# Kernel tuning notes

Hardware: AMD Instinct MI355X
Metric: run time of the kernel (lower is better)

The kernel has to match this reference:

```python
import jax, jax.numpy as jnp
import numpy as np

BATCH, N_FEATURES, D_MODEL = 8192, 8192, 1024


def setup_inputs() -> dict:
    key = jax.random.key(0)
    kx, kw = jax.random.split(key)
    # x: sparse feature activations in the original (COO); dense uniform here.
    x = jax.random.uniform(kx, (BATCH, N_FEATURES), dtype=jnp.float32)
    # Xavier-normal init for W_tr [n_features, d_model].
    std = float(np.sqrt(2.0 / (N_FEATURES + D_MODEL)))
    W_tr = jax.random.normal(kw, (N_FEATURES, D_MODEL), dtype=jnp.float32) * std
    bias = jnp.zeros((N_FEATURES,), dtype=jnp.float32)
    return {"x": x, "W_tr": W_tr, "bias": bias}


def reference(x, W_tr, bias):
    # h = x @ W_tr              : [B, n_features] @ [n_features, d_model] -> [B, d_model]
    # out = relu(h @ W_tr.T + b): [B, d_model] @ [d_model, n_features] -> [B, n_features]
    h = jnp.einsum("bf,fd->bd", x, W_tr)
    return jax.nn.relu(jnp.einsum("bd,fd->bf", h, W_tr) + bias)
```

## Files before the change

### kernel.cpp

```cpp
#include <hip/hip_runtime.h>
#include <hip/hip_bf16.h>
#include <stdint.h>

#define BATCH  8192
#define NFEAT  8192
#define DMODEL 1024

typedef unsigned short u16;
typedef __attribute__((ext_vector_type(8))) short  short8;
typedef __attribute__((ext_vector_type(4))) float  f32x4;

__device__ __forceinline__ u16 f2b(float f) {
    uint32_t u = __float_as_uint(f);
    u += 0x7fffu + ((u >> 16) & 1u);
    return (u16)(u >> 16);
}

__device__ __forceinline__ void gld16(const u16* g, void* l) {
    __builtin_amdgcn_global_load_lds(
        (const __attribute__((address_space(1))) void*)(uintptr_t)g,
        (__attribute__((address_space(3))) void*)(uint32_t)(uintptr_t)l,
        16, 0, 0);
}


__global__ void cvt_x_kernel(const float* __restrict__ x, u16* __restrict__ xb) {
    int i = blockIdx.x * blockDim.x + threadIdx.x;
    const float4* xv = (const float4*)x;
    float4 a = xv[2 * i];
    float4 b = xv[2 * i + 1];
    union { u16 u[8]; uint4 v; } o;
    o.u[0] = f2b(a.x); o.u[1] = f2b(a.y); o.u[2] = f2b(a.z); o.u[3] = f2b(a.w);
    o.u[4] = f2b(b.x); o.u[5] = f2b(b.y); o.u[6] = f2b(b.z); o.u[7] = f2b(b.w);
    ((uint4*)xb)[i] = o.v;
}

__global__ void cvt_w_kernel(const float* __restrict__ W,
                             u16* __restrict__ wb, u16* __restrict__ wt) {
    __shared__ u16 tile[64][65];
    const int f0 = blockIdx.x * 64;
    const int d0 = blockIdx.y * 64;
    const int t  = threadIdx.x;
#pragma unroll
    for (int rep = 0; rep < 16; ++rep) {
        int idx = rep * 256 + t;
        int r = idx >> 6, c = idx & 63;
        float v = W[(size_t)(f0 + r) * DMODEL + d0 + c];
        u16 u = f2b(v);
        tile[r][c] = u;
        wb[(size_t)(f0 + r) * DMODEL + d0 + c] = u;
    }
    __syncthreads();
#pragma unroll
    for (int rep = 0; rep < 16; ++rep) {
        int idx = rep * 256 + t;
        int r = idx >> 6, c = idx & 63;
        wt[(size_t)(d0 + r) * NFEAT + f0 + c] = tile[c][r];
    }
}

#define SYNC_IN()  do { __builtin_amdgcn_s_barrier(); \
                        asm volatile("s_waitcnt lgkmcnt(0)" ::: "memory"); } while (0)
#define SYNC_OUT() do { __builtin_amdgcn_s_setprio(0); __builtin_amdgcn_s_barrier(); } while (0)

__global__ __launch_bounds__(512, 2)
void gemm1_2ph(const u16* __restrict__ A, const u16* __restrict__ B,
               u16* __restrict__ H, int N, int K) {
    const int NT = K >> 6;
    __shared__ __align__(1024) char lds[131072];
    const int BOFF = 98304;

    const int tid  = threadIdx.x;
    const int lane = tid & 63;
    const int wave = tid >> 6;
    const int wm   = wave >> 2;
    const int wn   = wave & 3;

    const int nwg = gridDim.x;
    const int swz = (blockIdx.x & 7) * (nwg >> 3) + (blockIdx.x >> 3);
    const int ntn = N >> 7;
    const int tm0 = (swz / ntn) << 8;
    const int tn0 = (swz % ntn) << 7;

    const int srl = lane >> 2;
    const int sch = (lane & 3) ^ (((lane >> 5) & 1) << 1);
    const int scol  = (wave & 1) * 32 + sch * 8;
    const int srow0 = (wave >> 1) * 16 + srl;

    const u16* pa[2][2];
    pa[0][0] = A + (size_t)(tm0 + srow0)            * K + scol;
    pa[0][1] = A + (size_t)(tm0 + srow0 + 64)       * K + scol;
    pa[1][0] = A + (size_t)(tm0 + 128 + srow0)      * K + scol;
    pa[1][1] = A + (size_t)(tm0 + 128 + srow0 + 64) * K + scol;
    const u16* pb[2];
    pb[0] = B + (size_t)(tn0 + srow0)      * K + scol;
    pb[1] = B + (size_t)(tn0 + srow0 + 64) * K + scol;

    auto STAGE_A = [&](int tau, int half) {
        if (tau < NT) {
            char* d = lds + (tau % 3) * 32768 + half * 16384 + wave * 1024;
            gld16(pa[half][0] + (size_t)tau * 64, d);
            gld16(pa[half][1] + (size_t)tau * 64, d + 8192);
        }
    };
    auto STAGE_B = [&](int tau) {
        if (tau < NT) {
            char* d = lds + BOFF + (tau & 1) * 16384 + wave * 1024;
            gld16(pb[0] + (size_t)tau * 64, d);
            gld16(pb[1] + (size_t)tau * 64, d + 8192);
        }
    };

    const int l15 = lane & 15, lhi = lane >> 4;
    const int pch = lhi ^ (((lane >> 3) & 1) << 1);
    const int lof = l15 * 64 + pch * 16;

    short8 a[4][2];
    short8 b[2][2];
    f32x4  acc[8][2] = {};

    const char* Ab;
    const char* Bb;
    auto LDA_ = [&](int mh) {
#pragma unroll
        for (int fm = 0; fm < 4; ++fm)
#pragma unroll
            for (int ks = 0; ks < 2; ++ks)
                a[fm][ks] = *(const short8*)(Ab + ((mh * 4 + fm) * 2 + ks) * 1024);
    };
    auto LDB_ = [&](int nh) {
#pragma unroll
        for (int ks = 0; ks < 2; ++ks)
            b[nh][ks] = *(const short8*)(Bb + (nh * 2 + ks) * 1024);
    };
    auto MMA_ = [&](int mh, int nh) {
#pragma unroll
        for (int ks = 0; ks < 2; ++ks)
#pragma unroll
            for (int fm = 0; fm < 4; ++fm)
                acc[mh * 4 + fm][nh] = __builtin_amdgcn_mfma_f32_16x16x32_bf16(
                    a[fm][ks], b[nh][ks], acc[mh * 4 + fm][nh], 0, 0, 0);
    };

    STAGE_A(0, 0); STAGE_A(0, 1); STAGE_B(0);
    STAGE_A(1, 0); STAGE_A(1, 1); STAGE_B(1);
    asm volatile("s_waitcnt vmcnt(6)" ::: "memory");
    __builtin_amdgcn_s_barrier();

    for (int t = 0; t < NT; ++t) {
        Ab = lds + (t % 3) * 32768 + wm * 16384 + lof;
        Bb = lds + BOFF + (t & 1) * 16384 + wn * 4096 + lof;

        LDA_(0); LDB_(0); LDB_(1);
        STAGE_A(t + 2, 0);
        STAGE_A(t + 2, 1);
        SYNC_IN();
        __builtin_amdgcn_s_setprio(1);
        MMA_(0, 0);
        MMA_(0, 1);
        SYNC_OUT();

        LDA_(1);
        STAGE_B(t + 2);
        SYNC_IN();
        __builtin_amdgcn_s_setprio(1);
        MMA_(1, 1);
        MMA_(1, 0);
        __builtin_amdgcn_s_setprio(0);
        if (t < NT - 2)       asm volatile("s_waitcnt vmcnt(6)" ::: "memory");
        else if (t == NT - 2) asm volatile("s_waitcnt vmcnt(0)" ::: "memory");
        __builtin_amdgcn_s_barrier();
    }

    u16* lu = (u16*)lds;
#pragma unroll
    for (int fm = 0; fm < 8; ++fm)
#pragma unroll
        for (int nh = 0; nh < 2; ++nh) {
            const int col  = wn * 32 + nh * 16 + l15;
            const int row0 = wm * 128 + fm * 16 + lhi * 4;
#pragma unroll
            for (int r = 0; r < 4; ++r)
                lu[(row0 + r) * 128 + col] = f2b(acc[fm][nh][r]);
        }
    __syncthreads();
    const uint4* ls = (const uint4*)lds;
#pragma unroll
    for (int s = 0; s < 8; ++s) {
        int i = s * 512 + tid;
        int row = i >> 4;
        int col = (i & 15) * 8;
        *(uint4*)(H + (size_t)(tm0 + row) * N + (tn0 + col)) = ls[i];
    }
}

__global__ __launch_bounds__(512, 2)
void gemm2_persist(const u16* __restrict__ A, const u16* __restrict__ B,
                   float* __restrict__ O, const float* __restrict__ bias,
                   int N, int K) {
    __shared__ __align__(1024) char lds[163840];
    const int BOFF = 98304;
    const int TTOT = 64;

    const int tid  = threadIdx.x;
    const int lane = tid & 63;
    const int wave = tid >> 6;
    const int wm   = wave >> 2;
    const int wn   = wave & 3;

    const int bid = blockIdx.x;
    const int xcd = bid & 7;
    const int sub = (bid >> 3) & 3;
    const int mg  = bid >> 5;
    const int tn0     = ((xcd << 2) + sub) << 8;
    const int tm_base = mg << 10;

    const int srl = lane >> 2;
    const int sch = (lane & 3) ^ (((lane >> 5) & 1) << 1);
    const int scol  = (wave & 1) * 32 + sch * 8;
    const int srow0 = (wave >> 1) * 16 + srl;

    auto STAGE_A = [&](int tau, int half) {
        if (tau < TTOT) {
            char* d = lds + (tau % 3) * 32768 + half * 16384 + wave * 1024;
            const int rb = tm_base + ((tau >> 4) << 8) + half * 128 + srow0;
            const u16* p = A + (size_t)rb * K + ((tau & 15) << 6) + scol;
            gld16(p, d);
            gld16(p + (size_t)64 * K, d + 8192);
        }
    };
    auto STAGE_B = [&](int tau, int half) {
        if (tau < TTOT) {
            char* d = lds + BOFF + (tau & 1) * 32768 + half * 16384 + wave * 1024;
            const u16* p = B + (size_t)(tn0 + half * 128 + srow0) * K + ((tau & 15) << 6) + scol;
            gld16(p, d);
            gld16(p + (size_t)64 * K, d + 8192);
        }
    };

    const int l15 = lane & 15, lhi = lane >> 4;
    const int pch = lhi ^ (((lane >> 3) & 1) << 1);
    const int lof = l15 * 64 + pch * 16;

    short8 a[4][2];
    short8 b[4][2];
    f32x4  acc[8][4] = {};

    const char* Ab;
    const char* Bb;
    auto LDA_ = [&](int mh) {
#pragma unroll
        for (int fm = 0; fm < 4; ++fm)
#pragma unroll
            for (int ks = 0; ks < 2; ++ks)
                a[fm][ks] = *(const short8*)(Ab + ((mh * 4 + fm) * 2 + ks) * 1024);
    };
    auto LDB_ = [&](int nh) {
#pragma unroll
        for (int fn = 0; fn < 2; ++fn)
#pragma unroll
            for (int ks = 0; ks < 2; ++ks)
                b[nh * 2 + fn][ks] = *(const short8*)(Bb + (((wn & 1) * 4 + nh * 2 + fn) * 2 + ks) * 1024);
    };
    auto MMA_ = [&](int mh, int nh) {
#pragma unroll
        for (int ks = 0; ks < 2; ++ks)
#pragma unroll
            for (int fm = 0; fm < 4; ++fm)
#pragma unroll
                for (int fn = 0; fn < 2; ++fn)
                    acc[mh * 4 + fm][nh * 2 + fn] = __builtin_amdgcn_mfma_f32_16x16x32_bf16(
                        a[fm][ks], b[nh * 2 + fn][ks], acc[mh * 4 + fm][nh * 2 + fn], 0, 0, 0);
    };

    const int ocol = tn0 + wn * 64;
    float bv[4];
#pragma unroll
    for (int fn = 0; fn < 4; ++fn) bv[fn] = bias[ocol + fn * 16 + l15];

    STAGE_A(0, 0); STAGE_A(0, 1); STAGE_B(0, 0); STAGE_B(0, 1);
    STAGE_A(1, 0); STAGE_A(1, 1); STAGE_B(1, 0); STAGE_B(1, 1);
    asm volatile("s_waitcnt vmcnt(8)" ::: "memory");
    __builtin_amdgcn_s_barrier();

    for (int tt = 0; tt < TTOT; ++tt) {
        Ab = lds + (tt % 3) * 32768 + wm * 16384 + lof;
        Bb = lds + BOFF + (tt & 1) * 32768 + (wn >> 1) * 16384 + lof;

        LDA_(0); LDB_(0); LDB_(1);
        STAGE_A(tt + 2, 0);
        STAGE_A(tt + 2, 1);
        SYNC_IN();
        __builtin_amdgcn_s_setprio(1);
        MMA_(0, 0);
        MMA_(0, 1);
        SYNC_OUT();

        LDA_(1);
        STAGE_B(tt + 2, 0);
        STAGE_B(tt + 2, 1);
        SYNC_IN();
        __builtin_amdgcn_s_setprio(1);
        MMA_(1, 1);
        MMA_(1, 0);
        __builtin_amdgcn_s_setprio(0);
        if (tt < TTOT - 2)       asm volatile("s_waitcnt vmcnt(8)" ::: "memory");
        else if (tt == TTOT - 2) asm volatile("s_waitcnt vmcnt(0)" ::: "memory");
        __builtin_amdgcn_s_barrier();

        if ((tt & 15) == 15) {
            const int orow = tm_base + ((tt >> 4) << 8) + wm * 128;
#pragma unroll
            for (int fm = 0; fm < 8; ++fm) {
                const int row0 = orow + fm * 16 + lhi * 4;
#pragma unroll
                for (int fn = 0; fn < 4; ++fn) {
                    const int col = ocol + fn * 16 + l15;
#pragma unroll
                    for (int r = 0; r < 4; ++r) {
                        float v = acc[fm][fn][r] + bv[fn];
                        O[(size_t)(row0 + r) * N + col] = v > 0.f ? v : 0.f;
                        acc[fm][fn][r] = 0.f;
                    }
                }
            }
        }
    }
}


extern "C" void kernel_launch(void* const* d_in, const int* in_sizes, int n_in,
                              void* d_out, int out_size, void* d_ws, size_t ws_size,
                              hipStream_t stream) {
    const float* x    = (const float*)d_in[0];
    const float* W    = (const float*)d_in[1];
    const float* bias = (const float*)d_in[2];
    float* out = (float*)d_out;

    char* ws = (char*)d_ws;
    u16* xb = (u16*)ws;
    u16* wt = (u16*)(ws + 134217728);
    u16* wb = (u16*)(ws + 134217728 + 16777216);
    u16* hb = (u16*)(ws + 134217728 + 2 * 16777216);

    cvt_x_kernel<<<(BATCH * NFEAT / 8) / 256, 256, 0, stream>>>(x, xb);
    cvt_w_kernel<<<dim3(NFEAT / 64, DMODEL / 64), 256, 0, stream>>>(W, wb, wt);

    gemm1_2ph<<<dim3((BATCH / 256) * (DMODEL / 128)), 512, 0, stream>>>(
        xb, wt, hb, DMODEL, NFEAT);

    gemm2_persist<<<dim3(256), 512, 0, stream>>>(
        hb, wb, out, bias, NFEAT, DMODEL);
}
```

Measured before the change: 373.1 us.

## Restage GEMM tiles as full 128-byte rows with XOR-swizzled LDS chunks

Both GEMM kernels change how tiles are staged into LDS. Each group of 8 lanes now loads one full 64-element (128-byte) row per global-to-LDS load, instead of four lanes covering half a row. Rows are stored contiguously in LDS with the 16-byte chunk index XOR-swizzled by row, and the fragment reads use matching swizzled offsets. The aim is more coalesced global loads and bank-conflict-free LDS fragment reads, at the cost of different address arithmetic. The number of loads per stage is unchanged, so the vmcnt waits still match.

Result: no change. 379.0 us (+1.6%).

```diff
diff --git a/kernel.cpp b/kernel.cpp
--- a/kernel.cpp
+++ b/kernel.cpp
@@ -63,6 +63,7 @@
                         asm volatile("s_waitcnt lgkmcnt(0)" ::: "memory"); } while (0)
 #define SYNC_OUT() do { __builtin_amdgcn_s_setprio(0); __builtin_amdgcn_s_barrier(); } while (0)
 
+
 __global__ __launch_bounds__(512, 2)
 void gemm1_2ph(const u16* __restrict__ A, const u16* __restrict__ B,
                u16* __restrict__ H, int N, int K) {
@@ -82,38 +83,29 @@
     const int tm0 = (swz / ntn) << 8;
     const int tn0 = (swz % ntn) << 7;
 
-    const int srl = lane >> 2;
-    const int sch = (lane & 3) ^ (((lane >> 5) & 1) << 1);
-    const int scol  = (wave & 1) * 32 + sch * 8;
-    const int srow0 = (wave >> 1) * 16 + srl;
-
-    const u16* pa[2][2];
-    pa[0][0] = A + (size_t)(tm0 + srow0)            * K + scol;
-    pa[0][1] = A + (size_t)(tm0 + srow0 + 64)       * K + scol;
-    pa[1][0] = A + (size_t)(tm0 + 128 + srow0)      * K + scol;
-    pa[1][1] = A + (size_t)(tm0 + 128 + srow0 + 64) * K + scol;
-    const u16* pb[2];
-    pb[0] = B + (size_t)(tn0 + srow0)      * K + scol;
-    pb[1] = B + (size_t)(tn0 + srow0 + 64) * K + scol;
-
-    auto STAGE_A = [&](int tau, int half) {
+    const int sr8 = lane >> 3;
+    const int sg  = (lane & 7) ^ sr8;
+    const int l15 = lane & 15, lhi = lane >> 4;
+    const int ch0 = ((lhi ^ (lane & 7)) << 4);
+
+    auto STAGE_A = [&](int tau) {
         if (tau < NT) {
-            char* d = lds + (tau % 3) * 32768 + half * 16384 + wave * 1024;
-            gld16(pa[half][0] + (size_t)tau * 64, d);
-            gld16(pa[half][1] + (size_t)tau * 64, d + 8192);
+            char* d = lds + (tau % 3) * 32768 + wave * 4096;
+#pragma unroll
+            for (int i = 0; i < 4; ++i)
+                gld16(A + (size_t)(tm0 + wave * 32 + i * 8 + sr8) * K + ((size_t)tau << 6) + sg * 8,
+                      d + i * 1024);
         }
     };
     auto STAGE_B = [&](int tau) {
         if (tau < NT) {
-            char* d = lds + BOFF + (tau & 1) * 16384 + wave * 1024;
-            gld16(pb[0] + (size_t)tau * 64, d);
-            gld16(pb[1] + (size_t)tau * 64, d + 8192);
-        }
-    };
-
-    const int l15 = lane & 15, lhi = lane >> 4;
-    const int pch = lhi ^ (((lane >> 3) & 1) << 1);
-    const int lof = l15 * 64 + pch * 16;
+            char* d = lds + BOFF + (tau & 1) * 16384 + wave * 2048;
+#pragma unroll
+            for (int i = 0; i < 2; ++i)
+                gld16(B + (size_t)(tn0 + wave * 16 + i * 8 + sr8) * K + ((size_t)tau << 6) + sg * 8,
+                      d + i * 1024);
+        }
+    };
 
     short8 a[4][2];
     short8 b[2][2];
@@ -123,15 +115,14 @@
     const char* Bb;
     auto LDA_ = [&](int mh) {
 #pragma unroll
-        for (int fm = 0; fm < 4; ++fm)
-#pragma unroll
-            for (int ks = 0; ks < 2; ++ks)
-                a[fm][ks] = *(const short8*)(Ab + ((mh * 4 + fm) * 2 + ks) * 1024);
+        for (int fm = 0; fm < 4; ++fm) {
+            a[fm][0] = *(const short8*)(Ab + (mh * 4 + fm) * 2048 + ch0);
+            a[fm][1] = *(const short8*)(Ab + (mh * 4 + fm) * 2048 + (ch0 ^ 64));
+        }
     };
     auto LDB_ = [&](int nh) {
-#pragma unroll
-        for (int ks = 0; ks < 2; ++ks)
-            b[nh][ks] = *(const short8*)(Bb + (nh * 2 + ks) * 1024);
+        b[nh][0] = *(const short8*)(Bb + nh * 2048 + ch0);
+        b[nh][1] = *(const short8*)(Bb + nh * 2048 + (ch0 ^ 64));
     };
     auto MMA_ = [&](int mh, int nh) {
 #pragma unroll
@@ -142,18 +133,17 @@
                     a[fm][ks], b[nh][ks], acc[mh * 4 + fm][nh], 0, 0, 0);
     };
 
-    STAGE_A(0, 0); STAGE_A(0, 1); STAGE_B(0);
-    STAGE_A(1, 0); STAGE_A(1, 1); STAGE_B(1);
+    STAGE_A(0); STAGE_B(0);
+    STAGE_A(1); STAGE_B(1);
     asm volatile("s_waitcnt vmcnt(6)" ::: "memory");
     __builtin_amdgcn_s_barrier();
 
     for (int t = 0; t < NT; ++t) {
-        Ab = lds + (t % 3) * 32768 + wm * 16384 + lof;
-        Bb = lds + BOFF + (t & 1) * 16384 + wn * 4096 + lof;
+        Ab = lds + (t % 3) * 32768 + wm * 16384 + l15 * 128;
+        Bb = lds + BOFF + (t & 1) * 16384 + wn * 4096 + l15 * 128;
 
         LDA_(0); LDB_(0); LDB_(1);
-        STAGE_A(t + 2, 0);
-        STAGE_A(t + 2, 1);
+        STAGE_A(t + 2);
         SYNC_IN();
         __builtin_amdgcn_s_setprio(1);
         MMA_(0, 0);
@@ -215,32 +205,31 @@
     const int tn0     = ((xcd << 2) + sub) << 8;
     const int tm_base = mg << 10;
 
-    const int srl = lane >> 2;
-    const int sch = (lane & 3) ^ (((lane >> 5) & 1) << 1);
-    const int scol  = (wave & 1) * 32 + sch * 8;
-    const int srow0 = (wave >> 1) * 16 + srl;
-
-    auto STAGE_A = [&](int tau, int half) {
+    const int sr8 = lane >> 3;
+    const int sg  = (lane & 7) ^ sr8;
+    const int l15 = lane & 15, lhi = lane >> 4;
+    const int ch0 = ((lhi ^ (lane & 7)) << 4);
+
+    auto STAGE_A = [&](int tau) {
         if (tau < TTOT) {
-            char* d = lds + (tau % 3) * 32768 + half * 16384 + wave * 1024;
-            const int rb = tm_base + ((tau >> 4) << 8) + half * 128 + srow0;
-            const u16* p = A + (size_t)rb * K + ((tau & 15) << 6) + scol;
-            gld16(p, d);
-            gld16(p + (size_t)64 * K, d + 8192);
-        }
-    };
-    auto STAGE_B = [&](int tau, int half) {
+            char* d = lds + (tau % 3) * 32768 + wave * 4096;
+            const int rb = tm_base + ((tau >> 4) << 8) + wave * 32 + sr8;
+            const size_t co = ((size_t)(tau & 15) << 6) + sg * 8;
+#pragma unroll
+            for (int i = 0; i < 4; ++i)
+                gld16(A + (size_t)(rb + i * 8) * K + co, d + i * 1024);
+        }
+    };
+    auto STAGE_B = [&](int tau) {
         if (tau < TTOT) {
-            char* d = lds + BOFF + (tau & 1) * 32768 + half * 16384 + wave * 1024;
-            const u16* p = B + (size_t)(tn0 + half * 128 + srow0) * K + ((tau & 15) << 6) + scol;
-            gld16(p, d);
-            gld16(p + (size_t)64 * K, d + 8192);
-        }
-    };
-
-    const int l15 = lane & 15, lhi = lane >> 4;
-    const int pch = lhi ^ (((lane >> 3) & 1) << 1);
-    const int lof = l15 * 64 + pch * 16;
+            char* d = lds + BOFF + (tau & 1) * 32768 + wave * 4096;
+            const int rb = tn0 + wave * 32 + sr8;
+            const size_t co = ((size_t)(tau & 15) << 6) + sg * 8;
+#pragma unroll
+            for (int i = 0; i < 4; ++i)
+                gld16(B + (size_t)(rb + i * 8) * K + co, d + i * 1024);
+        }
+    };
 
     short8 a[4][2];
     short8 b[4][2];
@@ -250,17 +239,17 @@
     const char* Bb;
     auto LDA_ = [&](int mh) {
 #pragma unroll
-        for (int fm = 0; fm < 4; ++fm)
-#pragma unroll
-            for (int ks = 0; ks < 2; ++ks)
-                a[fm][ks] = *(const short8*)(Ab + ((mh * 4 + fm) * 2 + ks) * 1024);
+        for (int fm = 0; fm < 4; ++fm) {
+            a[fm][0] = *(const short8*)(Ab + (mh * 4 + fm) * 2048 + ch0);
+            a[fm][1] = *(const short8*)(Ab + (mh * 4 + fm) * 2048 + (ch0 ^ 64));
+        }
     };
     auto LDB_ = [&](int nh) {
 #pragma unroll
-        for (int fn = 0; fn < 2; ++fn)
-#pragma unroll
-            for (int ks = 0; ks < 2; ++ks)
-                b[nh * 2 + fn][ks] = *(const short8*)(Bb + (((wn & 1) * 4 + nh * 2 + fn) * 2 + ks) * 1024);
+        for (int fn = 0; fn < 2; ++fn) {
+            b[nh * 2 + fn][0] = *(const short8*)(Bb + (nh * 2 + fn) * 2048 + ch0);
+            b[nh * 2 + fn][1] = *(const short8*)(Bb + (nh * 2 + fn) * 2048 + (ch0 ^ 64));
+        }
     };
     auto MMA_ = [&](int mh, int nh) {
 #pragma unroll
@@ -278,18 +267,17 @@
 #pragma unroll
     for (int fn = 0; fn < 4; ++fn) bv[fn] = bias[ocol + fn * 16 + l15];
 
-    STAGE_A(0, 0); STAGE_A(0, 1); STAGE_B(0, 0); STAGE_B(0, 1);
-    STAGE_A(1, 0); STAGE_A(1, 1); STAGE_B(1, 0); STAGE_B(1, 1);
+    STAGE_A(0); STAGE_B(0);
+    STAGE_A(1); STAGE_B(1);
     asm volatile("s_waitcnt vmcnt(8)" ::: "memory");
     __builtin_amdgcn_s_barrier();
 
     for (int tt = 0; tt < TTOT; ++tt) {
-        Ab = lds + (tt % 3) * 32768 + wm * 16384 + lof;
-        Bb = lds + BOFF + (tt & 1) * 32768 + (wn >> 1) * 16384 + lof;
+        Ab = lds + (tt % 3) * 32768 + wm * 16384 + l15 * 128;
+        Bb = lds + BOFF + (tt & 1) * 32768 + wn * 8192 + l15 * 128;
 
         LDA_(0); LDB_(0); LDB_(1);
-        STAGE_A(tt + 2, 0);
-        STAGE_A(tt + 2, 1);
+        STAGE_A(tt + 2);
         SYNC_IN();
         __builtin_amdgcn_s_setprio(1);
         MMA_(0, 0);
@@ -297,8 +285,7 @@
         SYNC_OUT();
 
         LDA_(1);
-        STAGE_B(tt + 2, 0);
-        STAGE_B(tt + 2, 1);
+        STAGE_B(tt + 2);
         SYNC_IN();
         __builtin_amdgcn_s_setprio(1);
         MMA_(1, 1);
```
